# Kernel optimization log

Measured on AMD Instinct MI355X. Metric: run time of the kernel, lower is better.

## Reference

```python
import jax, jax.numpy as jnp
import numpy as np

N_NODES = 50000
N_EDGES = 800000
IN_FEATS = 128
H_FEATS = 128
NUM_CLASSES = 16


def setup_inputs() -> dict:
    key = jax.random.key(0)
    ks = jax.random.split(key, 10)
    in_feat = jax.random.normal(ks[0], (N_NODES, IN_FEATS), dtype=jnp.float32)
    src = jax.random.randint(ks[1], (N_EDGES,), 0, N_NODES, dtype=jnp.int64)
    dst = jax.random.randint(ks[2], (N_EDGES,), 0, N_NODES, dtype=jnp.int64)
    def glorot(k, shape):
        lim = np.sqrt(6.0 / (shape[0] + shape[1]))
        return jax.random.uniform(k, shape, jnp.float32, -lim, lim)
    W_self1 = glorot(ks[3], (IN_FEATS, H_FEATS))
    W_neigh1 = glorot(ks[4], (IN_FEATS, H_FEATS))
    b1 = jnp.zeros((H_FEATS,), jnp.float32)
    W_self2 = glorot(ks[5], (H_FEATS, NUM_CLASSES))
    W_neigh2 = glorot(ks[6], (H_FEATS, NUM_CLASSES))
    b2 = jnp.zeros((NUM_CLASSES,), jnp.float32)
    return {"in_feat": in_feat, "src": src, "dst": dst,
            "W_self1": W_self1, "W_neigh1": W_neigh1, "b1": b1,
            "W_self2": W_self2, "W_neigh2": W_neigh2, "b2": b2}


def _mean_agg(h, src, dst, n_nodes):
    # sum of source features at each destination node, divided by in-degree
    summed = jax.ops.segment_sum(h[src], dst, num_segments=n_nodes)  # [N, d]
    deg = jax.ops.segment_sum(jnp.ones_like(dst, dtype=h.dtype), dst,
                              num_segments=n_nodes)                   # [N]
    return summed / jnp.maximum(deg, 1.0)[:, None]


def _sage_conv(h, src, dst, W_self, W_neigh, b):
    h_neigh = _mean_agg(h, src, dst, h.shape[0])
    return h @ W_self + h_neigh @ W_neigh + b


def reference(in_feat, src, dst, W_self1, W_neigh1, b1, W_self2, W_neigh2, b2):
    h = _sage_conv(in_feat, src, dst, W_self1, W_neigh1, b1)
    h = jax.nn.relu(h)
    h = _sage_conv(h, src, dst, W_self2, W_neigh2, b2)
    return h
```

## Files before the change

### kernel.cpp

```cpp
#include <hip/hip_runtime.h>

#define NF 128
#define BSH 8
#define CHUNK 4096

typedef __attribute__((ext_vector_type(8))) short short8;
typedef __attribute__((ext_vector_type(4))) float floatx4;

__device__ __forceinline__ unsigned short f2bf(float f) {
    unsigned u = __float_as_uint(f);
    u += 0x7fff + ((u >> 16) & 1);
    return (unsigned short)(u >> 16);
}
__device__ __forceinline__ unsigned pk2(float a, float b) {
    return (unsigned)f2bf(a) | ((unsigned)f2bf(b) << 16);
}
__device__ __forceinline__ float bflo(unsigned u) { return __uint_as_float(u << 16); }
__device__ __forceinline__ float bfhi(unsigned u) { return __uint_as_float(u & 0xffff0000u); }

__device__ __forceinline__ unsigned enc8(float f) {
    unsigned b = __float_as_uint(f);
    unsigned s = (b >> 24) & 0x80u;
    b &= 0x7fffffffu;
    unsigned t = b + 0x7FFFFu + ((b >> 20) & 1u);
    unsigned m = (t >= 0x3C800000u) ? (((t - 0x3C000000u) >> 20) & 0x7Fu) : 0u;
    return s | m;
}
__device__ __forceinline__ void dec4(float* acc, unsigned w) {
#pragma unroll
    for (int j = 0; j < 4; ++j) {
        unsigned u = (w >> (8 * j)) & 0xffu;
        acc[j] += __uint_as_float(((u & 0x80u) << 24) | ((u & 0x7fu) << 20));
    }
}


__global__ __launch_bounds__(256) void k_prep(const float* __restrict__ in_feat,
                                              const int* __restrict__ dst,
                                              const float* __restrict__ Ws1,
                                              const float* __restrict__ Wn1,
                                              const float* __restrict__ Ws2,
                                              const float* __restrict__ Wn2,
                                              unsigned short* __restrict__ featbf,
                                              unsigned char* __restrict__ feat8,
                                              unsigned short* __restrict__ W1t,
                                              unsigned short* __restrict__ W2t,
                                              int* __restrict__ gcnt,
                                              int nb_cvt, int nb_w, int E) {
    int b = blockIdx.x, tid = threadIdx.x;
    if (b < nb_cvt) {
        int i = b * 256 + tid;
        const float4* p = (const float4*)in_feat + (size_t)i * 2;
        float4 a = p[0], c = p[1];
        uint4 o;
        o.x = pk2(a.x, a.y); o.y = pk2(a.z, a.w);
        o.z = pk2(c.x, c.y); o.w = pk2(c.z, c.w);
        ((uint4*)featbf)[i] = o;
        uint2 q;
        q.x = enc8(a.x) | (enc8(a.y) << 8) | (enc8(a.z) << 16) | (enc8(a.w) << 24);
        q.y = enc8(c.x) | (enc8(c.y) << 8) | (enc8(c.z) << 16) | (enc8(c.w) << 24);
        ((uint2*)feat8)[i] = q;
    } else if (b < nb_cvt + nb_w) {
        int idx = (b - nb_cvt) * 256 + tid;
        if (idx < 128 * 256) {
            int n = idx >> 8, kk = idx & 255;
            float v = (kk < 128) ? Ws1[(size_t)kk * 128 + n]
                                 : Wn1[(size_t)(kk - 128) * 128 + n];
            W1t[idx] = f2bf(v);
        } else {
            int idx2 = idx - 128 * 256;
            if (idx2 < 32 * 128) {
                int n = idx2 >> 7, k = idx2 & 127;
                float v = (n < 16) ? Ws2[(size_t)k * 16 + n]
                                   : Wn2[(size_t)k * 16 + (n - 16)];
                W2t[idx2] = f2bf(v);
            }
        }
    } else {
        __shared__ int h[256];
        h[tid] = 0;
        __syncthreads();
        int base = (b - nb_cvt - nb_w) * CHUNK;
        int n = min(CHUNK, E - base);
        for (int i = tid; i < n; i += 256) atomicAdd(&h[dst[base + i] >> BSH], 1);
        __syncthreads();
        if (h[tid]) atomicAdd(&gcnt[tid], h[tid]);
    }
}


__global__ __launch_bounds__(256) void k_cscan(const int* __restrict__ gcnt,
                                               int* __restrict__ goff,
                                               int* __restrict__ gcur) {
    __shared__ int sw[4];
    int tid = threadIdx.x, lane = tid & 63, w = tid >> 6;
    int v = gcnt[tid], inc = v;
#pragma unroll
    for (int d = 1; d < 64; d <<= 1) {
        int t = __shfl_up(inc, (unsigned)d, 64);
        if (lane >= d) inc += t;
    }
    if (lane == 63) sw[w] = inc;
    __syncthreads();
    int add = 0;
    for (int i = 0; i < w; ++i) add += sw[i];
    int ex = add + inc - v;
    goff[tid] = ex;
    gcur[tid] = ex;
    if (tid == 255) goff[256] = ex + v;
}


__global__ __launch_bounds__(256) void k_part(const int* __restrict__ src,
                                              const int* __restrict__ dst,
                                              int* __restrict__ gcur,
                                              unsigned* __restrict__ ebuf, int E) {
    __shared__ int h[256];
    __shared__ int basep[256];
    int tid = threadIdx.x;
    h[tid] = 0;
    __syncthreads();
    int base = blockIdx.x * CHUNK;
    int n = min(CHUNK, E - base);
    for (int i = tid; i < n; i += 256) atomicAdd(&h[dst[base + i] >> BSH], 1);
    __syncthreads();
    basep[tid] = h[tid] ? atomicAdd(&gcur[tid], h[tid]) : 0;
    h[tid] = 0;
    __syncthreads();
    for (int i = tid; i < n; i += 256) {
        int dd = dst[base + i];
        int bk = dd >> BSH;
        int p = basep[bk] + atomicAdd(&h[bk], 1);
        ebuf[p] = ((unsigned)(dd & 255) << 16) | (unsigned)src[base + i];
    }
}


__global__ __launch_bounds__(256) void k_fine(const unsigned* __restrict__ ebuf,
                                              const int* __restrict__ goff,
                                              int* __restrict__ off,
                                              int* __restrict__ csr, int N) {
    __shared__ int degL[256];
    __shared__ int offL[256];
    __shared__ int sw[4];
    int b = blockIdx.x, tid = threadIdx.x;
    int node0 = b << BSH;
    int e0 = goff[b], e1 = goff[b + 1];
    degL[tid] = 0;
    __syncthreads();
    for (int e = e0 + tid; e < e1; e += 256) atomicAdd(&degL[ebuf[e] >> 16], 1);
    __syncthreads();
    int lane = tid & 63, w = tid >> 6;
    int v = degL[tid], inc = v;
#pragma unroll
    for (int d = 1; d < 64; d <<= 1) {
        int t = __shfl_up(inc, (unsigned)d, 64);
        if (lane >= d) inc += t;
    }
    if (lane == 63) sw[w] = inc;
    __syncthreads();
    int add = 0;
    for (int i = 0; i < w; ++i) add += sw[i];
    int ex = add + inc - v;
    offL[tid] = ex;
    int idx = node0 + tid;
    if (idx <= N) off[idx] = e0 + ex;
    degL[tid] = 0;
    __syncthreads();
    for (int e = e0 + tid; e < e1; e += 256) {
        unsigned u = ebuf[e];
        int d = u >> 16;
        int pos = e0 + offL[d] + atomicAdd(&degL[d], 1);
        csr[pos] = (int)(u & 0xffffu);
    }
}


__global__ __launch_bounds__(256) void k_agg1(const unsigned char* __restrict__ feat8,
                                              const int* __restrict__ off,
                                              const int* __restrict__ csr,
                                              unsigned short* __restrict__ outm, int N) {
    int idx = blockIdx.x * 256 + threadIdx.x;
    int g = idx >> 3;
    int lane = idx & 7;
    if (g >= N) return;
    int s0 = off[g], s1 = off[g + 1];
    float acc[16];
#pragma unroll
    for (int i = 0; i < 16; ++i) acc[i] = 0.f;
    const uint4* F = (const uint4*)feat8;
    int e = s0;
    for (; e + 3 < s1; e += 4) {
        int sA = csr[e], sB = csr[e + 1], sC = csr[e + 2], sD = csr[e + 3];
        uint4 va = F[(size_t)sA * 8 + lane];
        uint4 vb = F[(size_t)sB * 8 + lane];
        uint4 vc = F[(size_t)sC * 8 + lane];
        uint4 vd = F[(size_t)sD * 8 + lane];
        dec4(acc + 0, va.x); dec4(acc + 4, va.y); dec4(acc + 8, va.z); dec4(acc + 12, va.w);
        dec4(acc + 0, vb.x); dec4(acc + 4, vb.y); dec4(acc + 8, vb.z); dec4(acc + 12, vb.w);
        dec4(acc + 0, vc.x); dec4(acc + 4, vc.y); dec4(acc + 8, vc.z); dec4(acc + 12, vc.w);
        dec4(acc + 0, vd.x); dec4(acc + 4, vd.y); dec4(acc + 8, vd.z); dec4(acc + 12, vd.w);
    }
    for (; e < s1; ++e) {
        int s = csr[e];
        uint4 va = F[(size_t)s * 8 + lane];
        dec4(acc + 0, va.x); dec4(acc + 4, va.y); dec4(acc + 8, va.z); dec4(acc + 12, va.w);
    }
    float inv = __uint_as_float(0x7B800000u) / fmaxf((float)(s1 - s0), 1.0f);
    uint4 o0, o1;
    o0.x = pk2(acc[0] * inv, acc[1] * inv);
    o0.y = pk2(acc[2] * inv, acc[3] * inv);
    o0.z = pk2(acc[4] * inv, acc[5] * inv);
    o0.w = pk2(acc[6] * inv, acc[7] * inv);
    o1.x = pk2(acc[8] * inv, acc[9] * inv);
    o1.y = pk2(acc[10] * inv, acc[11] * inv);
    o1.z = pk2(acc[12] * inv, acc[13] * inv);
    o1.w = pk2(acc[14] * inv, acc[15] * inv);
    uint4* op = (uint4*)(outm + (size_t)g * NF + lane * 16);
    op[0] = o0;
    op[1] = o1;
}


__global__ __launch_bounds__(256) void k_gemm1(const unsigned short* __restrict__ Abf,
                                               const unsigned short* __restrict__ Hbf,
                                               const unsigned short* __restrict__ Wt,
                                               const float* __restrict__ bias,
                                               unsigned short* __restrict__ out, int M) {
    int tid = threadIdx.x;
    int w = tid >> 6, lane = tid & 63;
    int q = lane >> 4, r = lane & 15;
    int row = blockIdx.x * 64 + w * 16 + r;
    int rowc = min(row, M - 1);

    floatx4 acc[8];
#pragma unroll
    for (int t = 0; t < 8; ++t) acc[t] = (floatx4){0.f, 0.f, 0.f, 0.f};

    const unsigned short* arow = Abf + (size_t)rowc * 128;
    const unsigned short* hrow = Hbf + (size_t)rowc * 128;

#pragma unroll
    for (int kc = 0; kc < 8; ++kc) {
        const unsigned short* ap = (kc < 4) ? (arow + kc * 32 + q * 8)
                                            : (hrow + (kc - 4) * 32 + q * 8);
        short8 a = *(const short8*)ap;
        const unsigned short* wp = Wt + kc * 32 + q * 8 + (size_t)r * 256;
#pragma unroll
        for (int t = 0; t < 8; ++t) {
            short8 b = *(const short8*)(wp + (size_t)t * 16 * 256);
            acc[t] = __builtin_amdgcn_mfma_f32_16x16x32_bf16(a, b, acc[t], 0, 0, 0);
        }
    }

    int orow0 = blockIdx.x * 64 + w * 16 + q * 4;
#pragma unroll
    for (int i = 0; i < 4; ++i) {
        int orow = orow0 + i;
        if (orow < M) {
            unsigned short* op = out + (size_t)orow * 128;
#pragma unroll
            for (int t = 0; t < 8; ++t) {
                float v = fmaxf(acc[t][i] + bias[t * 16 + r], 0.0f);
                op[t * 16 + r] = f2bf(v);
            }
        }
    }
}


__global__ __launch_bounds__(256) void k_gemm2(const unsigned short* __restrict__ Abf,
                                               const unsigned short* __restrict__ Wt,
                                               const float* __restrict__ bias,
                                               float* __restrict__ t2s,
                                               unsigned short* __restrict__ t2n, int M) {
    int tid = threadIdx.x;
    int w = tid >> 6, lane = tid & 63;
    int q = lane >> 4, r = lane & 15;
    int row = blockIdx.x * 64 + w * 16 + r;
    int rowc = min(row, M - 1);

    floatx4 acc[2];
#pragma unroll
    for (int t = 0; t < 2; ++t) acc[t] = (floatx4){0.f, 0.f, 0.f, 0.f};

    const unsigned short* arow = Abf + (size_t)rowc * 128;

#pragma unroll
    for (int kc = 0; kc < 4; ++kc) {
        short8 a = *(const short8*)(arow + kc * 32 + q * 8);
        const unsigned short* wp = Wt + kc * 32 + q * 8 + (size_t)r * 128;
#pragma unroll
        for (int t = 0; t < 2; ++t) {
            short8 b = *(const short8*)(wp + (size_t)t * 16 * 128);
            acc[t] = __builtin_amdgcn_mfma_f32_16x16x32_bf16(a, b, acc[t], 0, 0, 0);
        }
    }

    int orow0 = blockIdx.x * 64 + w * 16 + q * 4;
    float b0 = bias[r];
#pragma unroll
    for (int i = 0; i < 4; ++i) {
        int orow = orow0 + i;
        if (orow < M) {
            t2s[(size_t)orow * 16 + r] = acc[0][i] + b0;
            t2n[(size_t)orow * 16 + r] = f2bf(acc[1][i]);
        }
    }
}


__global__ __launch_bounds__(256) void k_out(const float* __restrict__ t2s,
                                             const unsigned short* __restrict__ t2n,
                                             const int* __restrict__ off,
                                             const int* __restrict__ csr,
                                             float* __restrict__ out, int N) {
    int idx = blockIdx.x * 256 + threadIdx.x;
    int node = idx >> 1;
    if (node >= N) return;
    int ln = idx & 1;
    int s0 = off[node], s1 = off[node + 1];
    float acc[8];
#pragma unroll
    for (int i = 0; i < 8; ++i) acc[i] = 0.f;
    const uint4* T = (const uint4*)t2n;
    int e = s0;
    for (; e + 3 < s1; e += 4) {
        int sA = csr[e], sB = csr[e + 1], sC = csr[e + 2], sD = csr[e + 3];
        uint4 va = T[(size_t)sA * 2 + ln];
        uint4 vb = T[(size_t)sB * 2 + ln];
        uint4 vc = T[(size_t)sC * 2 + ln];
        uint4 vd = T[(size_t)sD * 2 + ln];
        acc[0] += bflo(va.x) + bflo(vb.x) + bflo(vc.x) + bflo(vd.x);
        acc[1] += bfhi(va.x) + bfhi(vb.x) + bfhi(vc.x) + bfhi(vd.x);
        acc[2] += bflo(va.y) + bflo(vb.y) + bflo(vc.y) + bflo(vd.y);
        acc[3] += bfhi(va.y) + bfhi(vb.y) + bfhi(vc.y) + bfhi(vd.y);
        acc[4] += bflo(va.z) + bflo(vb.z) + bflo(vc.z) + bflo(vd.z);
        acc[5] += bfhi(va.z) + bfhi(vb.z) + bfhi(vc.z) + bfhi(vd.z);
        acc[6] += bflo(va.w) + bflo(vb.w) + bflo(vc.w) + bflo(vd.w);
        acc[7] += bfhi(va.w) + bfhi(vb.w) + bfhi(vc.w) + bfhi(vd.w);
    }
    for (; e < s1; ++e) {
        int s = csr[e];
        uint4 va = T[(size_t)s * 2 + ln];
        acc[0] += bflo(va.x); acc[1] += bfhi(va.x);
        acc[2] += bflo(va.y); acc[3] += bfhi(va.y);
        acc[4] += bflo(va.z); acc[5] += bfhi(va.z);
        acc[6] += bflo(va.w); acc[7] += bfhi(va.w);
    }
    float inv = 1.0f / fmaxf((float)(s1 - s0), 1.0f);
    const float4* sp = (const float4*)(t2s + (size_t)node * 16 + ln * 8);
    float4 sa = sp[0], sb = sp[1];
    float4 r0, r1;
    r0.x = sa.x + acc[0] * inv; r0.y = sa.y + acc[1] * inv;
    r0.z = sa.z + acc[2] * inv; r0.w = sa.w + acc[3] * inv;
    r1.x = sb.x + acc[4] * inv; r1.y = sb.y + acc[5] * inv;
    r1.z = sb.z + acc[6] * inv; r1.w = sb.w + acc[7] * inv;
    float4* op = (float4*)(out + (size_t)node * 16 + ln * 8);
    op[0] = r0;
    op[1] = r1;
}


extern "C" void kernel_launch(void* const* d_in, const int* in_sizes, int n_in,
                              void* d_out, int out_size, void* d_ws, size_t ws_size,
                              hipStream_t stream) {
    const float* in_feat = (const float*)d_in[0];
    const int*   src     = (const int*)d_in[1];
    const int*   dst     = (const int*)d_in[2];
    const float* Ws1     = (const float*)d_in[3];
    const float* Wn1     = (const float*)d_in[4];
    const float* b1      = (const float*)d_in[5];
    const float* Ws2     = (const float*)d_in[6];
    const float* Wn2     = (const float*)d_in[7];
    const float* b2      = (const float*)d_in[8];
    float* outp = (float*)d_out;

    int N = in_sizes[0] / NF;
    int E = in_sizes[1];
    int nb = (N + 255) >> BSH;

    char* ws = (char*)d_ws;
    size_t o = 0;
    auto alloc = [&](size_t bytes) -> char* {
        char* p = ws + o;
        o = (o + bytes + 255) & ~(size_t)255;
        return p;
    };
    int*      gcnt = (int*)alloc(256 * 4);
    int*      goff = (int*)alloc(257 * 4);
    int*      gcur = (int*)alloc(256 * 4);
    int*      off  = (int*)alloc((size_t)(N + 1) * 4);
    int*      csr  = (int*)alloc((size_t)E * 4);
    unsigned* ebuf = (unsigned*)alloc((size_t)E * 4);
    unsigned short* featbf = (unsigned short*)alloc((size_t)N * NF * 2);
    unsigned char*  feat8  = (unsigned char*)alloc((size_t)N * NF);
    unsigned short* hn1    = (unsigned short*)alloc((size_t)N * NF * 2);
    unsigned short* h1     = (unsigned short*)alloc((size_t)N * NF * 2);
    unsigned short* W1t    = (unsigned short*)alloc((size_t)128 * 256 * 2);
    unsigned short* W2t    = (unsigned short*)alloc((size_t)32 * 128 * 2);
    float*          t2s    = (float*)alloc((size_t)N * 16 * 4);
    unsigned short* t2n    = (unsigned short*)alloc((size_t)N * 16 * 2);

    hipMemsetAsync(gcnt, 0, 256 * 4, stream);

    int nb_cvt = (N * NF / 8 + 255) / 256;
    int nb_w = (128 * 256 + 32 * 128 + 255) / 256;
    int nb_cc = (E + CHUNK - 1) / CHUNK;
    k_prep<<<nb_cvt + nb_w + nb_cc, 256, 0, stream>>>(in_feat, dst, Ws1, Wn1, Ws2, Wn2,
                                                      featbf, feat8, W1t, W2t, gcnt,
                                                      nb_cvt, nb_w, E);
    k_cscan<<<1, 256, 0, stream>>>(gcnt, goff, gcur);
    k_part<<<nb_cc, 256, 0, stream>>>(src, dst, gcur, ebuf, E);
    k_fine<<<nb, 256, 0, stream>>>(ebuf, goff, off, csr, N);

    k_agg1<<<(N * 8 + 255) / 256, 256, 0, stream>>>(feat8, off, csr, hn1, N);

    int gb_m = (N + 63) / 64;
    k_gemm1<<<gb_m, 256, 0, stream>>>(featbf, hn1, W1t, b1, h1, N);
    k_gemm2<<<gb_m, 256, 0, stream>>>(h1, W2t, b2, t2s, t2n, N);
    k_out<<<(N * 2 + 255) / 256, 256, 0, stream>>>(t2s, t2n, off, csr, outp, N);
}
```

Before: 219.9 us.

## Fuse both GEMMs, store per-chunk histograms, unroll layer-1 gather by eight

Layer-1 and layer-2 GEMMs are merged into one kernel that stages the ReLU'd hidden tile in shared memory and runs the second MFMA from it. This removes the h1 round trip through global memory and one launch. The partition step now stores a per-chunk bucket histogram in k_prep, and a single-block scan computes per-chunk base offsets. k_part can then skip recounting and global atomics, at the cost of a serial scan over all chunks in one block. The layer-1 aggregation gather loop is also unrolled from four to eight edges, giving more loads in flight per thread.

Result: slower. 252.9 us (+15.0%).

```diff
diff --git a/kernel.cpp b/kernel.cpp
--- a/kernel.cpp
+++ b/kernel.cpp
@@ -45,7 +45,7 @@
                                               unsigned char* __restrict__ feat8,
                                               unsigned short* __restrict__ W1t,
                                               unsigned short* __restrict__ W2t,
-                                              int* __restrict__ gcnt,
+                                              int* __restrict__ cnt2,
                                               int nb_cvt, int nb_w, int E) {
     int b = blockIdx.x, tid = threadIdx.x;
     if (b < nb_cvt) {
@@ -78,23 +78,35 @@
         }
     } else {
         __shared__ int h[256];
+        int c = b - nb_cvt - nb_w;
         h[tid] = 0;
         __syncthreads();
-        int base = (b - nb_cvt - nb_w) * CHUNK;
+        int base = c * CHUNK;
         int n = min(CHUNK, E - base);
         for (int i = tid; i < n; i += 256) atomicAdd(&h[dst[base + i] >> BSH], 1);
         __syncthreads();
-        if (h[tid]) atomicAdd(&gcnt[tid], h[tid]);
-    }
-}
-
-
-__global__ __launch_bounds__(256) void k_cscan(const int* __restrict__ gcnt,
+        cnt2[c * 256 + tid] = h[tid];
+    }
+}
+
+
+__global__ __launch_bounds__(256) void k_cscan(const int* __restrict__ cnt2,
                                                int* __restrict__ goff,
-                                               int* __restrict__ gcur) {
+                                               int* __restrict__ basep, int nc) {
     __shared__ int sw[4];
     int tid = threadIdx.x, lane = tid & 63, w = tid >> 6;
-    int v = gcnt[tid], inc = v;
+    int tot = 0;
+    int c = 0;
+    for (; c + 7 < nc; c += 8) {
+        int v0 = cnt2[(c + 0) * 256 + tid], v1 = cnt2[(c + 1) * 256 + tid];
+        int v2 = cnt2[(c + 2) * 256 + tid], v3 = cnt2[(c + 3) * 256 + tid];
+        int v4 = cnt2[(c + 4) * 256 + tid], v5 = cnt2[(c + 5) * 256 + tid];
+        int v6 = cnt2[(c + 6) * 256 + tid], v7 = cnt2[(c + 7) * 256 + tid];
+        tot += ((v0 + v1) + (v2 + v3)) + ((v4 + v5) + (v6 + v7));
+    }
+    for (; c < nc; ++c) tot += cnt2[c * 256 + tid];
+
+    int inc = tot;
 #pragma unroll
     for (int d = 1; d < 64; d <<= 1) {
         int t = __shfl_up(inc, (unsigned)d, 64);
@@ -104,33 +116,38 @@
     __syncthreads();
     int add = 0;
     for (int i = 0; i < w; ++i) add += sw[i];
-    int ex = add + inc - v;
+    int ex = add + inc - tot;
     goff[tid] = ex;
-    gcur[tid] = ex;
-    if (tid == 255) goff[256] = ex + v;
+    if (tid == 255) goff[256] = ex + tot;
+
+    int run = ex;
+    for (c = 0; c < nc; c += 8) {
+        int v[8];
+#pragma unroll
+        for (int j = 0; j < 8; ++j)
+            v[j] = (c + j < nc) ? cnt2[(c + j) * 256 + tid] : 0;
+#pragma unroll
+        for (int j = 0; j < 8; ++j) {
+            if (c + j < nc) basep[(c + j) * 256 + tid] = run;
+            run += v[j];
+        }
+    }
 }
 
 
 __global__ __launch_bounds__(256) void k_part(const int* __restrict__ src,
                                               const int* __restrict__ dst,
-                                              int* __restrict__ gcur,
+                                              const int* __restrict__ basep,
                                               unsigned* __restrict__ ebuf, int E) {
-    __shared__ int h[256];
-    __shared__ int basep[256];
+    __shared__ int cur[256];
     int tid = threadIdx.x;
-    h[tid] = 0;
+    cur[tid] = basep[blockIdx.x * 256 + tid];
     __syncthreads();
     int base = blockIdx.x * CHUNK;
     int n = min(CHUNK, E - base);
-    for (int i = tid; i < n; i += 256) atomicAdd(&h[dst[base + i] >> BSH], 1);
-    __syncthreads();
-    basep[tid] = h[tid] ? atomicAdd(&gcur[tid], h[tid]) : 0;
-    h[tid] = 0;
-    __syncthreads();
     for (int i = tid; i < n; i += 256) {
         int dd = dst[base + i];
-        int bk = dd >> BSH;
-        int p = basep[bk] + atomicAdd(&h[bk], 1);
+        int p = atomicAdd(&cur[dd >> BSH], 1);
         ebuf[p] = ((unsigned)(dd & 255) << 16) | (unsigned)src[base + i];
     }
 }
@@ -190,20 +207,26 @@
     for (int i = 0; i < 16; ++i) acc[i] = 0.f;
     const uint4* F = (const uint4*)feat8;
     int e = s0;
-    for (; e + 3 < s1; e += 4) {
-        int sA = csr[e], sB = csr[e + 1], sC = csr[e + 2], sD = csr[e + 3];
-        uint4 va = F[(size_t)sA * 8 + lane];
-        uint4 vb = F[(size_t)sB * 8 + lane];
-        uint4 vc = F[(size_t)sC * 8 + lane];
-        uint4 vd = F[(size_t)sD * 8 + lane];
-        dec4(acc + 0, va.x); dec4(acc + 4, va.y); dec4(acc + 8, va.z); dec4(acc + 12, va.w);
-        dec4(acc + 0, vb.x); dec4(acc + 4, vb.y); dec4(acc + 8, vb.z); dec4(acc + 12, vb.w);
-        dec4(acc + 0, vc.x); dec4(acc + 4, vc.y); dec4(acc + 8, vc.z); dec4(acc + 12, vc.w);
-        dec4(acc + 0, vd.x); dec4(acc + 4, vd.y); dec4(acc + 8, vd.z); dec4(acc + 12, vd.w);
+    for (; e + 7 < s1; e += 8) {
+        uint4 v0 = F[(size_t)csr[e + 0] * 8 + lane];
+        uint4 v1 = F[(size_t)csr[e + 1] * 8 + lane];
+        uint4 v2 = F[(size_t)csr[e + 2] * 8 + lane];
+        uint4 v3 = F[(size_t)csr[e + 3] * 8 + lane];
+        uint4 v4 = F[(size_t)csr[e + 4] * 8 + lane];
+        uint4 v5 = F[(size_t)csr[e + 5] * 8 + lane];
+        uint4 v6 = F[(size_t)csr[e + 6] * 8 + lane];
+        uint4 v7 = F[(size_t)csr[e + 7] * 8 + lane];
+        dec4(acc + 0, v0.x); dec4(acc + 4, v0.y); dec4(acc + 8, v0.z); dec4(acc + 12, v0.w);
+        dec4(acc + 0, v1.x); dec4(acc + 4, v1.y); dec4(acc + 8, v1.z); dec4(acc + 12, v1.w);
+        dec4(acc + 0, v2.x); dec4(acc + 4, v2.y); dec4(acc + 8, v2.z); dec4(acc + 12, v2.w);
+        dec4(acc + 0, v3.x); dec4(acc + 4, v3.y); dec4(acc + 8, v3.z); dec4(acc + 12, v3.w);
+        dec4(acc + 0, v4.x); dec4(acc + 4, v4.y); dec4(acc + 8, v4.z); dec4(acc + 12, v4.w);
+        dec4(acc + 0, v5.x); dec4(acc + 4, v5.y); dec4(acc + 8, v5.z); dec4(acc + 12, v5.w);
+        dec4(acc + 0, v6.x); dec4(acc + 4, v6.y); dec4(acc + 8, v6.z); dec4(acc + 12, v6.w);
+        dec4(acc + 0, v7.x); dec4(acc + 4, v7.y); dec4(acc + 8, v7.z); dec4(acc + 12, v7.w);
     }
     for (; e < s1; ++e) {
-        int s = csr[e];
-        uint4 va = F[(size_t)s * 8 + lane];
+        uint4 va = F[(size_t)csr[e] * 8 + lane];
         dec4(acc + 0, va.x); dec4(acc + 4, va.y); dec4(acc + 8, va.z); dec4(acc + 12, va.w);
     }
     float inv = __uint_as_float(0x7B800000u) / fmaxf((float)(s1 - s0), 1.0f);
@@ -222,11 +245,15 @@
 }
 
 
-__global__ __launch_bounds__(256) void k_gemm1(const unsigned short* __restrict__ Abf,
-                                               const unsigned short* __restrict__ Hbf,
-                                               const unsigned short* __restrict__ Wt,
-                                               const float* __restrict__ bias,
-                                               unsigned short* __restrict__ out, int M) {
+__global__ __launch_bounds__(256) void k_gemm(const unsigned short* __restrict__ Abf,
+                                              const unsigned short* __restrict__ Hbf,
+                                              const unsigned short* __restrict__ W1t,
+                                              const float* __restrict__ b1,
+                                              const unsigned short* __restrict__ W2t,
+                                              const float* __restrict__ b2,
+                                              float* __restrict__ t2s,
+                                              unsigned short* __restrict__ t2n, int M) {
+    __shared__ float hL[64 * 140];
     int tid = threadIdx.x;
     int w = tid >> 6, lane = tid & 63;
     int q = lane >> 4, r = lane & 15;
@@ -245,7 +272,7 @@
         const unsigned short* ap = (kc < 4) ? (arow + kc * 32 + q * 8)
                                             : (hrow + (kc - 4) * 32 + q * 8);
         short8 a = *(const short8*)ap;
-        const unsigned short* wp = Wt + kc * 32 + q * 8 + (size_t)r * 256;
+        const unsigned short* wp = W1t + kc * 32 + q * 8 + (size_t)r * 256;
 #pragma unroll
         for (int t = 0; t < 8; ++t) {
             short8 b = *(const short8*)(wp + (size_t)t * 16 * 256);
@@ -253,58 +280,42 @@
         }
     }
 
+#pragma unroll
+    for (int i = 0; i < 4; ++i) {
+        int lr = w * 16 + q * 4 + i;
+#pragma unroll
+        for (int t = 0; t < 8; ++t)
+            hL[lr * 140 + t * 16 + r] = fmaxf(acc[t][i] + b1[t * 16 + r], 0.0f);
+    }
+
+    floatx4 acc2[2];
+#pragma unroll
+    for (int t = 0; t < 2; ++t) acc2[t] = (floatx4){0.f, 0.f, 0.f, 0.f};
+
+#pragma unroll
+    for (int kc = 0; kc < 4; ++kc) {
+        const float* pa = hL + (w * 16 + r) * 140 + kc * 32 + q * 8;
+        float4 fa = *(const float4*)pa;
+        float4 fb = *(const float4*)(pa + 4);
+        union { short8 s; uint4 u; } cv;
+        cv.u = make_uint4(pk2(fa.x, fa.y), pk2(fa.z, fa.w),
+                          pk2(fb.x, fb.y), pk2(fb.z, fb.w));
+        const unsigned short* wp = W2t + kc * 32 + q * 8 + (size_t)r * 128;
+#pragma unroll
+        for (int t = 0; t < 2; ++t) {
+            short8 b = *(const short8*)(wp + (size_t)t * 16 * 128);
+            acc2[t] = __builtin_amdgcn_mfma_f32_16x16x32_bf16(cv.s, b, acc2[t], 0, 0, 0);
+        }
+    }
+
     int orow0 = blockIdx.x * 64 + w * 16 + q * 4;
+    float bb = b2[r];
 #pragma unroll
     for (int i = 0; i < 4; ++i) {
         int orow = orow0 + i;
         if (orow < M) {
-            unsigned short* op = out + (size_t)orow * 128;
-#pragma unroll
-            for (int t = 0; t < 8; ++t) {
-                float v = fmaxf(acc[t][i] + bias[t * 16 + r], 0.0f);
-                op[t * 16 + r] = f2bf(v);
-            }
-        }
-    }
-}
-
-
-__global__ __launch_bounds__(256) void k_gemm2(const unsigned short* __restrict__ Abf,
-                                               const unsigned short* __restrict__ Wt,
-                                               const float* __restrict__ bias,
-                                               float* __restrict__ t2s,
-                                               unsigned short* __restrict__ t2n, int M) {
-    int tid = threadIdx.x;
-    int w = tid >> 6, lane = tid & 63;
-    int q = lane >> 4, r = lane & 15;
-    int row = blockIdx.x * 64 + w * 16 + r;
-    int rowc = min(row, M - 1);
-
-    floatx4 acc[2];
-#pragma unroll
-    for (int t = 0; t < 2; ++t) acc[t] = (floatx4){0.f, 0.f, 0.f, 0.f};
-
-    const unsigned short* arow = Abf + (size_t)rowc * 128;
-
-#pragma unroll
-    for (int kc = 0; kc < 4; ++kc) {
-        short8 a = *(const short8*)(arow + kc * 32 + q * 8);
-        const unsigned short* wp = Wt + kc * 32 + q * 8 + (size_t)r * 128;
-#pragma unroll
-        for (int t = 0; t < 2; ++t) {
-            short8 b = *(const short8*)(wp + (size_t)t * 16 * 128);
-            acc[t] = __builtin_amdgcn_mfma_f32_16x16x32_bf16(a, b, acc[t], 0, 0, 0);
-        }
-    }
-
-    int orow0 = blockIdx.x * 64 + w * 16 + q * 4;
-    float b0 = bias[r];
-#pragma unroll
-    for (int i = 0; i < 4; ++i) {
-        int orow = orow0 + i;
-        if (orow < M) {
-            t2s[(size_t)orow * 16 + r] = acc[0][i] + b0;
-            t2n[(size_t)orow * 16 + r] = f2bf(acc[1][i]);
+            t2s[(size_t)orow * 16 + r] = acc2[0][i] + bb;
+            t2n[(size_t)orow * 16 + r] = f2bf(acc2[1][i]);
         }
     }
 }
@@ -326,11 +337,10 @@
     const uint4* T = (const uint4*)t2n;
     int e = s0;
     for (; e + 3 < s1; e += 4) {
-        int sA = csr[e], sB = csr[e + 1], sC = csr[e + 2], sD = csr[e + 3];
-        uint4 va = T[(size_t)sA * 2 + ln];
-        uint4 vb = T[(size_t)sB * 2 + ln];
-        uint4 vc = T[(size_t)sC * 2 + ln];
-        uint4 vd = T[(size_t)sD * 2 + ln];
+        uint4 va = T[(size_t)csr[e + 0] * 2 + ln];
+        uint4 vb = T[(size_t)csr[e + 1] * 2 + ln];
+        uint4 vc = T[(size_t)csr[e + 2] * 2 + ln];
+        uint4 vd = T[(size_t)csr[e + 3] * 2 + ln];
         acc[0] += bflo(va.x) + bflo(vb.x) + bflo(vc.x) + bflo(vd.x);
         acc[1] += bfhi(va.x) + bfhi(vb.x) + bfhi(vc.x) + bfhi(vd.x);
         acc[2] += bflo(va.y) + bflo(vb.y) + bflo(vc.y) + bflo(vd.y);
@@ -341,8 +351,7 @@
         acc[7] += bfhi(va.w) + bfhi(vb.w) + bfhi(vc.w) + bfhi(vd.w);
     }
     for (; e < s1; ++e) {
-        int s = csr[e];
-        uint4 va = T[(size_t)s * 2 + ln];
+        uint4 va = T[(size_t)csr[e] * 2 + ln];
         acc[0] += bflo(va.x); acc[1] += bfhi(va.x);
         acc[2] += bflo(va.y); acc[3] += bfhi(va.y);
         acc[4] += bflo(va.z); acc[5] += bfhi(va.z);
@@ -379,6 +388,7 @@
     int N = in_sizes[0] / NF;
     int E = in_sizes[1];
     int nb = (N + 255) >> BSH;
+    int nc = (E + CHUNK - 1) / CHUNK;
 
     char* ws = (char*)d_ws;
     size_t o = 0;
@@ -387,37 +397,32 @@
         o = (o + bytes + 255) & ~(size_t)255;
         return p;
     };
-    int*      gcnt = (int*)alloc(256 * 4);
-    int*      goff = (int*)alloc(257 * 4);
-    int*      gcur = (int*)alloc(256 * 4);
-    int*      off  = (int*)alloc((size_t)(N + 1) * 4);
-    int*      csr  = (int*)alloc((size_t)E * 4);
-    unsigned* ebuf = (unsigned*)alloc((size_t)E * 4);
+    int*      cnt2  = (int*)alloc((size_t)nc * 256 * 4);
+    int*      basep = (int*)alloc((size_t)nc * 256 * 4);
+    int*      goff  = (int*)alloc(257 * 4);
+    int*      off   = (int*)alloc((size_t)(N + 1) * 4);
+    int*      csr   = (int*)alloc((size_t)E * 4);
+    unsigned* ebuf  = (unsigned*)alloc((size_t)E * 4);
     unsigned short* featbf = (unsigned short*)alloc((size_t)N * NF * 2);
     unsigned char*  feat8  = (unsigned char*)alloc((size_t)N * NF);
     unsigned short* hn1    = (unsigned short*)alloc((size_t)N * NF * 2);
-    unsigned short* h1     = (unsigned short*)alloc((size_t)N * NF * 2);
     unsigned short* W1t    = (unsigned short*)alloc((size_t)128 * 256 * 2);
     unsigned short* W2t    = (unsigned short*)alloc((size_t)32 * 128 * 2);
     float*          t2s    = (float*)alloc((size_t)N * 16 * 4);
     unsigned short* t2n    = (unsigned short*)alloc((size_t)N * 16 * 2);
 
-    hipMemsetAsync(gcnt, 0, 256 * 4, stream);
-
     int nb_cvt = (N * NF / 8 + 255) / 256;
     int nb_w = (128 * 256 + 32 * 128 + 255) / 256;
-    int nb_cc = (E + CHUNK - 1) / CHUNK;
-    k_prep<<<nb_cvt + nb_w + nb_cc, 256, 0, stream>>>(in_feat, dst, Ws1, Wn1, Ws2, Wn2,
-                                                      featbf, feat8, W1t, W2t, gcnt,
-                                                      nb_cvt, nb_w, E);
-    k_cscan<<<1, 256, 0, stream>>>(gcnt, goff, gcur);
-    k_part<<<nb_cc, 256, 0, stream>>>(src, dst, gcur, ebuf, E);
+    k_prep<<<nb_cvt + nb_w + nc, 256, 0, stream>>>(in_feat, dst, Ws1, Wn1, Ws2, Wn2,
+                                                   featbf, feat8, W1t, W2t, cnt2,
+                                                   nb_cvt, nb_w, E);
+    k_cscan<<<1, 256, 0, stream>>>(cnt2, goff, basep, nc);
+    k_part<<<nc, 256, 0, stream>>>(src, dst, basep, ebuf, E);
     k_fine<<<nb, 256, 0, stream>>>(ebuf, goff, off, csr, N);
 
     k_agg1<<<(N * 8 + 255) / 256, 256, 0, stream>>>(feat8, off, csr, hn1, N);
 
     int gb_m = (N + 63) / 64;
-    k_gemm1<<<gb_m, 256, 0, stream>>>(featbf, hn1, W1t, b1, h1, N);
-    k_gemm2<<<gb_m, 256, 0, stream>>>(h1, W2t, b2, t2s, t2n, N);
+    k_gemm<<<gb_m, 256, 0, stream>>>(featbf, hn1, W1t, b1, W2t, b2, t2s, t2n, N);
     k_out<<<(N * 2 + 255) / 256, 256, 0, stream>>>(t2s, t2n, off, csr, outp, N);
 }
```
